# Optimization experiments

Hardware: AMD Instinct MI355X
Metric: run time of the kernel (lower is better)

Reference implementation:

```python
import jax, jax.numpy as jnp
import numpy as np


def setup_inputs() -> dict:
    key = jax.random.key(0)
    k1, k2 = jax.random.split(key)
    B, C, H, W = 8, 64, 128, 256
    src = jax.random.normal(k1, (B, C, H, W), dtype=jnp.float32)
    tgt = jax.random.normal(k2, (B, C, H, W), dtype=jnp.float32)
    return {"src": src, "tgt": tgt, "search_range": 4}


def reference(src, tgt, search_range):
    # Cost volume: for each (dy, dx) shift of tgt (zero-padded), channel dot with src.
    # Output channel ordering matches the torch loop: center, then for i=1..S:
    # (+i,0), (-i,0), (0,+i), (0,-i), then for j=1..S: (+i,+j), (-i,+j), (+i,-j), (-i,-j).
    S = search_range
    B, C, H, W = src.shape
    tgt_pad = jnp.pad(tgt, ((0, 0), (0, 0), (S, S), (S, S)))

    def cost(di, dj):
        # shifted[y, x] = tgt[y - di, x - dj] (zero outside)
        shifted = tgt_pad[:, :, S - di:S - di + H, S - dj:S - dj + W]
        return jnp.sum(shifted * src, axis=1)  # [B, H, W]

    outs = [cost(0, 0)]
    for i in range(1, S + 1):
        outs.extend([cost(i, 0), cost(-i, 0), cost(0, i), cost(0, -i)])
        for j in range(1, S + 1):
            outs.extend([cost(i, j), cost(-i, j), cost(i, -j), cost(-i, -j)])
    return jnp.stack(outs, axis=1)  # [B, (2S+1)^2, H, W]
```

## Files before the change

### kernel.cpp

```cpp
#include <hip/hip_runtime.h>

#define S    4
#define BB   8
#define CC   64
#define HH   128
#define WW   256
#define KCH  8
#define NCP  4
#define TH   4
#define TW   64
#define PX   4
#define NTX  16
#define TROWS 12
#define PITCHD 72
#define SPITCH 64
#define NT   576
#define NCH  (CC / KCH)
#define HW   (HH * WW)
#define TGTU (NCP * TROWS * 18)
#define SRCU (NCP * TH * 16)
#define L2SZ (NCP * TROWS * PITCHD)
#define LSSZ (NCP * TH * SPITCH)

typedef _Float16 h2 __attribute__((ext_vector_type(2)));

__device__ inline h2 pack2(float x, float y) {
  return __builtin_bit_cast(h2, __builtin_amdgcn_cvt_pkrtz(x, y));
}
__device__ inline float dot2(h2 a, h2 b, float c) {
  return __builtin_amdgcn_fdot2(a, b, c, false);
}

__device__ __host__ constexpr int ord_idx(int di, int dj) {
  int i = di < 0 ? -di : di;
  int j = dj < 0 ? -dj : dj;
  if (i == 0 && j == 0) return 0;
  if (j == 0) return 1 + (i - 1) * 20 + (di > 0 ? 0 : 1);
  if (i == 0) return 1 + (j - 1) * 20 + (dj > 0 ? 2 : 3);
  return 1 + (i - 1) * 20 + 4 + (j - 1) * 4 +
         (di > 0 ? (dj > 0 ? 0 : 2) : (dj > 0 ? 1 : 3));
}

__device__ inline void lds_barrier() {
  asm volatile("s_waitcnt lgkmcnt(0)" ::: "memory");
  __builtin_amdgcn_s_barrier();
  __builtin_amdgcn_sched_barrier(0);
}

__global__ __launch_bounds__(NT, 4)
void costvol_kernel(const float* __restrict__ src,
                    const float* __restrict__ tgt,
                    float* __restrict__ out) {
  __shared__ __align__(16) float lds2[2][L2SZ];
  __shared__ __align__(16) float ldss[2][LSSZ];

  const int tx  = threadIdx.x;
  const int ty  = threadIdx.y;
  const int tz  = threadIdx.z;
  const int tid = tz * 64 + ty * 16 + tx;
  const int bx  = blockIdx.x;
  const int by  = blockIdx.y;
  const int b   = blockIdx.z;

  const int w0b = bx * TW;
  const int h0  = by * TH;
  const int h   = h0 + ty;
  const int w0  = w0b + tx * PX;
  const int di  = tz - S;
  const int row = ty - tz + 8;

  int lofs0 = -1, goff0 = -1, lofs1 = -1, goff1 = -1;
#pragma unroll
  for (int k = 0; k < 2; ++k) {
    const int u = tid + k * NT;
    if (u < TGTU) {
      const int cp  = u / (TROWS * 18);
      const int rem = u - cp * (TROWS * 18);
      const int r   = rem / 18;
      const int wq  = rem - r * 18;
      const int gh  = h0 - S + r;
      const int gw  = w0b - S + 4 * wq;
      const int lo  = cp * (TROWS * PITCHD) + r * PITCHD + 4 * wq;
      int go = -1;
      if ((unsigned)gh < (unsigned)HH && gw >= 0 && gw + 3 < WW)
        go = ((b * CC + 2 * cp) * HW) + gh * WW + gw;
      if (k == 0) { lofs0 = lo; goff0 = go; } else { lofs1 = lo; goff1 = go; }
    }
  }

  const int scp = (tid >> 6) & 3;
  const int sr  = (tid >> 4) & 3;
  const int sq  = tid & 15;
  const int sgo = (b * CC + 2 * scp) * HW + (h0 + sr) * WW + w0b + 4 * sq;
  const int slo = (scp * TH + sr) * SPITCH + 4 * sq;

  float acc[9][PX];
#pragma unroll
  for (int o = 0; o < 9; ++o)
#pragma unroll
    for (int p = 0; p < PX; ++p) acc[o][p] = 0.f;

  float4 tA0, tB0, tA1, tB1, sA, sB;
  const float4 z4 = make_float4(0.f, 0.f, 0.f, 0.f);

#define ISSUE(CHN) do {                                                     \
    const int _off = (CHN) * (KCH * HW);                                    \
    tA0 = z4; tB0 = z4; tA1 = z4; tB1 = z4;                                 \
    if (goff0 >= 0) {                                                       \
      tA0 = *reinterpret_cast<const float4*>(tgt + goff0 + _off);           \
      tB0 = *reinterpret_cast<const float4*>(tgt + goff0 + _off + HW);      \
    }                                                                       \
    if (goff1 >= 0) {                                                       \
      tA1 = *reinterpret_cast<const float4*>(tgt + goff1 + _off);           \
      tB1 = *reinterpret_cast<const float4*>(tgt + goff1 + _off + HW);      \
    }                                                                       \
    if (tid < SRCU) {                                                       \
      sA = *reinterpret_cast<const float4*>(src + sgo + _off);              \
      sB = *reinterpret_cast<const float4*>(src + sgo + _off + HW);         \
    }                                                                       \
  } while (0)

#define PACKQ(VA, VB, DST) do {                                             \
    float4 _wv;                                                             \
    _wv.x = __builtin_bit_cast(float, pack2((VA).x, (VB).x));               \
    _wv.y = __builtin_bit_cast(float, pack2((VA).y, (VB).y));               \
    _wv.z = __builtin_bit_cast(float, pack2((VA).z, (VB).z));               \
    _wv.w = __builtin_bit_cast(float, pack2((VA).w, (VB).w));               \
    *reinterpret_cast<float4*>(DST) = _wv;                                  \
  } while (0)

  ISSUE(0);

  int s = 0;
  for (int ch = 0; ch < NCH; ++ch) {
    float* lb2w = &lds2[0][0] + s * L2SZ;
    float* lbsw = &ldss[0][0] + s * LSSZ;
    if (lofs0 >= 0) PACKQ(tA0, tB0, lb2w + lofs0);
    if (lofs1 >= 0) PACKQ(tA1, tB1, lb2w + lofs1);
    if (tid < SRCU) PACKQ(sA, sB, lbsw + slo);

    if (ch + 1 < NCH) ISSUE(ch + 1);

    lds_barrier();

    const float* lb2 = &lds2[0][0] + s * L2SZ;
    const float* lbs = &ldss[0][0] + s * LSSZ;
#pragma unroll
    for (int cp = 0; cp < NCP; ++cp) {
      const float4 st = *reinterpret_cast<const float4*>(
          lbs + (cp * TH + ty) * SPITCH + 4 * tx);
      const h2 sv[PX] = {__builtin_bit_cast(h2, st.x), __builtin_bit_cast(h2, st.y),
                         __builtin_bit_cast(h2, st.z), __builtin_bit_cast(h2, st.w)};

      const float* lp = lb2 + cp * (TROWS * PITCHD) + row * PITCHD + 4 * tx;
      h2 win[12];
#pragma unroll
      for (int q = 0; q < 3; ++q) {
        const float4 t = *reinterpret_cast<const float4*>(lp + 4 * q);
        win[4 * q]     = __builtin_bit_cast(h2, t.x);
        win[4 * q + 1] = __builtin_bit_cast(h2, t.y);
        win[4 * q + 2] = __builtin_bit_cast(h2, t.z);
        win[4 * q + 3] = __builtin_bit_cast(h2, t.w);
      }

#pragma unroll
      for (int dj = -S; dj <= S; ++dj) {
#pragma unroll
        for (int p = 0; p < PX; ++p)
          acc[dj + S][p] = dot2(sv[p], win[p - dj + 4], acc[dj + S][p]);
      }
    }

    s ^= 1;
  }

  const size_t HWs = (size_t)HW;
  float* op = out + (size_t)b * 81 * HWs + (size_t)h * WW + w0;
#pragma unroll
  for (int dj = -S; dj <= S; ++dj) {
    const int o    = ord_idx(di, dj);
    const int slot = dj + S;
    *reinterpret_cast<float4*>(op + (size_t)o * HWs) =
        make_float4(acc[slot][0], acc[slot][1], acc[slot][2], acc[slot][3]);
  }
}

extern "C" void kernel_launch(void* const* d_in, const int* in_sizes, int n_in,
                              void* d_out, int out_size, void* d_ws, size_t ws_size,
                              hipStream_t stream) {
  const float* src = (const float*)d_in[0];
  const float* tgt = (const float*)d_in[1];
  float* out = (float*)d_out;
  dim3 grid(WW / TW, HH / TH, BB);
  dim3 block(NTX, TH, 9);
  costvol_kernel<<<grid, block, 0, stream>>>(src, tgt, out);
}
```

Measured before the change: 65.55 us.

## Halve grid and loop each block over two row tiles

The 3D grid of 1024 blocks becomes a flat grid of 512 blocks. Each block decodes batch, column tile and a base row tile from its linear id, then handles two row tiles 16 tiles apart in sequence, reusing the same double-buffered LDS pipeline. The intent is to cut block launch and setup cost and spread work more evenly across CUs. In exchange, fewer blocks are resident per CU, so there is less parallelism for latency hiding, and each block's two tiles run back to back with no overlap between them.

```diff
diff --git a/kernel.cpp b/kernel.cpp
--- a/kernel.cpp
+++ b/kernel.cpp
@@ -58,18 +58,19 @@
   const int ty  = threadIdx.y;
   const int tz  = threadIdx.z;
   const int tid = tz * 64 + ty * 16 + tx;
-  const int bx  = blockIdx.x;
-  const int by  = blockIdx.y;
-  const int b   = blockIdx.z;
+
+  const int bid = blockIdx.x;
+  const int b   = bid >> 6;
+  const int bx  = bid & 3;
+  const int by0 = (bid >> 2) & 15;
 
   const int w0b = bx * TW;
-  const int h0  = by * TH;
-  const int h   = h0 + ty;
   const int w0  = w0b + tx * PX;
   const int di  = tz - S;
   const int row = ty - tz + 8;
 
-  int lofs0 = -1, goff0 = -1, lofs1 = -1, goff1 = -1;
+  int lofs0 = -1, gb0 = 0, r0 = 0; bool gwok0 = false;
+  int lofs1 = -1, gb1 = 0, r1 = 0; bool gwok1 = false;
 #pragma unroll
   for (int k = 0; k < 2; ++k) {
     const int u = tid + k * NT;
@@ -78,27 +79,20 @@
       const int rem = u - cp * (TROWS * 18);
       const int r   = rem / 18;
       const int wq  = rem - r * 18;
-      const int gh  = h0 - S + r;
       const int gw  = w0b - S + 4 * wq;
       const int lo  = cp * (TROWS * PITCHD) + r * PITCHD + 4 * wq;
-      int go = -1;
-      if ((unsigned)gh < (unsigned)HH && gw >= 0 && gw + 3 < WW)
-        go = ((b * CC + 2 * cp) * HW) + gh * WW + gw;
-      if (k == 0) { lofs0 = lo; goff0 = go; } else { lofs1 = lo; goff1 = go; }
+      const bool ok = (gw >= 0 && gw + 3 < WW);
+      const int gb  = (b * CC + 2 * cp) * HW + (r - S) * WW + gw;
+      if (k == 0) { lofs0 = lo; gb0 = gb; r0 = r; gwok0 = ok; }
+      else        { lofs1 = lo; gb1 = gb; r1 = r; gwok1 = ok; }
     }
   }
 
   const int scp = (tid >> 6) & 3;
   const int sr  = (tid >> 4) & 3;
   const int sq  = tid & 15;
-  const int sgo = (b * CC + 2 * scp) * HW + (h0 + sr) * WW + w0b + 4 * sq;
-  const int slo = (scp * TH + sr) * SPITCH + 4 * sq;
-
-  float acc[9][PX];
-#pragma unroll
-  for (int o = 0; o < 9; ++o)
-#pragma unroll
-    for (int p = 0; p < PX; ++p) acc[o][p] = 0.f;
+  const int sbase = (b * CC + 2 * scp) * HW + sr * WW + w0b + 4 * sq;
+  const int slo   = (scp * TH + sr) * SPITCH + 4 * sq;
 
   float4 tA0, tB0, tA1, tB1, sA, sB;
   const float4 z4 = make_float4(0.f, 0.f, 0.f, 0.f);
@@ -129,59 +123,78 @@
     *reinterpret_cast<float4*>(DST) = _wv;                                  \
   } while (0)
 
-  ISSUE(0);
-
-  int s = 0;
-  for (int ch = 0; ch < NCH; ++ch) {
-    float* lb2w = &lds2[0][0] + s * L2SZ;
-    float* lbsw = &ldss[0][0] + s * LSSZ;
-    if (lofs0 >= 0) PACKQ(tA0, tB0, lb2w + lofs0);
-    if (lofs1 >= 0) PACKQ(tA1, tB1, lb2w + lofs1);
-    if (tid < SRCU) PACKQ(sA, sB, lbsw + slo);
-
-    if (ch + 1 < NCH) ISSUE(ch + 1);
-
-    lds_barrier();
-
-    const float* lb2 = &lds2[0][0] + s * L2SZ;
-    const float* lbs = &ldss[0][0] + s * LSSZ;
-#pragma unroll
-    for (int cp = 0; cp < NCP; ++cp) {
-      const float4 st = *reinterpret_cast<const float4*>(
-          lbs + (cp * TH + ty) * SPITCH + 4 * tx);
-      const h2 sv[PX] = {__builtin_bit_cast(h2, st.x), __builtin_bit_cast(h2, st.y),
-                         __builtin_bit_cast(h2, st.z), __builtin_bit_cast(h2, st.w)};
-
-      const float* lp = lb2 + cp * (TROWS * PITCHD) + row * PITCHD + 4 * tx;
-      h2 win[12];
-#pragma unroll
-      for (int q = 0; q < 3; ++q) {
-        const float4 t = *reinterpret_cast<const float4*>(lp + 4 * q);
-        win[4 * q]     = __builtin_bit_cast(h2, t.x);
-        win[4 * q + 1] = __builtin_bit_cast(h2, t.y);
-        win[4 * q + 2] = __builtin_bit_cast(h2, t.z);
-        win[4 * q + 3] = __builtin_bit_cast(h2, t.w);
+#pragma unroll 1
+  for (int t = 0; t < 2; ++t) {
+    const int h0 = (by0 + 16 * t) * TH;
+    const int h  = h0 + ty;
+
+    int goff0 = -1, goff1 = -1;
+    if (lofs0 >= 0 && gwok0 && (unsigned)(h0 - S + r0) < (unsigned)HH)
+      goff0 = gb0 + h0 * WW;
+    if (lofs1 >= 0 && gwok1 && (unsigned)(h0 - S + r1) < (unsigned)HH)
+      goff1 = gb1 + h0 * WW;
+    const int sgo = sbase + h0 * WW;
+
+    float acc[9][PX];
+#pragma unroll
+    for (int o = 0; o < 9; ++o)
+#pragma unroll
+      for (int p = 0; p < PX; ++p) acc[o][p] = 0.f;
+
+    ISSUE(0);
+
+    int s = 0;
+    for (int ch = 0; ch < NCH; ++ch) {
+      float* lb2w = &lds2[0][0] + s * L2SZ;
+      float* lbsw = &ldss[0][0] + s * LSSZ;
+      if (lofs0 >= 0) PACKQ(tA0, tB0, lb2w + lofs0);
+      if (lofs1 >= 0) PACKQ(tA1, tB1, lb2w + lofs1);
+      if (tid < SRCU) PACKQ(sA, sB, lbsw + slo);
+
+      if (ch + 1 < NCH) ISSUE(ch + 1);
+
+      lds_barrier();
+
+      const float* lb2 = &lds2[0][0] + s * L2SZ;
+      const float* lbs = &ldss[0][0] + s * LSSZ;
+#pragma unroll
+      for (int cp = 0; cp < NCP; ++cp) {
+        const float4 st = *reinterpret_cast<const float4*>(
+            lbs + (cp * TH + ty) * SPITCH + 4 * tx);
+        const h2 sv[PX] = {__builtin_bit_cast(h2, st.x), __builtin_bit_cast(h2, st.y),
+                           __builtin_bit_cast(h2, st.z), __builtin_bit_cast(h2, st.w)};
+
+        const float* lp = lb2 + cp * (TROWS * PITCHD) + row * PITCHD + 4 * tx;
+        h2 win[12];
+#pragma unroll
+        for (int q = 0; q < 3; ++q) {
+          const float4 tq = *reinterpret_cast<const float4*>(lp + 4 * q);
+          win[4 * q]     = __builtin_bit_cast(h2, tq.x);
+          win[4 * q + 1] = __builtin_bit_cast(h2, tq.y);
+          win[4 * q + 2] = __builtin_bit_cast(h2, tq.z);
+          win[4 * q + 3] = __builtin_bit_cast(h2, tq.w);
+        }
+
+#pragma unroll
+        for (int dj = -S; dj <= S; ++dj) {
+#pragma unroll
+          for (int p = 0; p < PX; ++p)
+            acc[dj + S][p] = dot2(sv[p], win[p - dj + 4], acc[dj + S][p]);
+        }
       }
 
-#pragma unroll
-      for (int dj = -S; dj <= S; ++dj) {
-#pragma unroll
-        for (int p = 0; p < PX; ++p)
-          acc[dj + S][p] = dot2(sv[p], win[p - dj + 4], acc[dj + S][p]);
-      }
+      s ^= 1;
     }
 
-    s ^= 1;
-  }
-
-  const size_t HWs = (size_t)HW;
-  float* op = out + (size_t)b * 81 * HWs + (size_t)h * WW + w0;
-#pragma unroll
-  for (int dj = -S; dj <= S; ++dj) {
-    const int o    = ord_idx(di, dj);
-    const int slot = dj + S;
-    *reinterpret_cast<float4*>(op + (size_t)o * HWs) =
-        make_float4(acc[slot][0], acc[slot][1], acc[slot][2], acc[slot][3]);
+    const size_t HWs = (size_t)HW;
+    float* op = out + (size_t)b * 81 * HWs + (size_t)h * WW + w0;
+#pragma unroll
+    for (int dj = -S; dj <= S; ++dj) {
+      const int o    = ord_idx(di, dj);
+      const int slot = dj + S;
+      *reinterpret_cast<float4*>(op + (size_t)o * HWs) =
+          make_float4(acc[slot][0], acc[slot][1], acc[slot][2], acc[slot][3]);
+    }
   }
 }
 
@@ -191,7 +204,7 @@
   const float* src = (const float*)d_in[0];
   const float* tgt = (const float*)d_in[1];
   float* out = (float*)d_out;
-  dim3 grid(WW / TW, HH / TH, BB);
+  dim3 grid(512, 1, 1);
   dim3 block(NTX, TH, 9);
   costvol_kernel<<<grid, block, 0, stream>>>(src, tgt, out);
 }
```

Measured after the change: 66.88 us. 2.0% more time.
